# Kernel optimization log

Measured on AMD Instinct MI355X. Metric: run time of the kernel, lower is better.

## Reference

```python
import jax, jax.numpy as jnp
import numpy as np

EMBED_SIZE = 2048
EBS = 512            # embed_block_size
NB = EMBED_SIZE // EBS  # num_blocks = 4
HEADS = 8
HD = EBS // HEADS    # head_dim = 64
N, S = 4, 1024


def block_linear(x, W, b):
    # x: [T, NB, EBS], W: [NB, EBS, EBS], b: [NB, EBS]
    return jnp.einsum('tbi,bio->tbo', x, W) + b


def setup_inputs() -> dict:
    key = jax.random.key(0)
    ks = jax.random.split(key, 11)
    sc = 1.0 / np.sqrt(EBS)
    inp = {
        'values': jax.random.normal(ks[0], (N, S, EMBED_SIZE), jnp.float32),
        'keys': jax.random.normal(ks[1], (N, S, EMBED_SIZE), jnp.float32),
        'query': jax.random.normal(ks[2], (N, S, EMBED_SIZE), jnp.float32),
        'mask': jnp.ones((N, 1, 1, S, S), jnp.int32),
        'Wv': jax.random.normal(ks[3], (NB, EBS, EBS), jnp.float32) * sc,
        'bv': jnp.zeros((NB, EBS), jnp.float32),
        'Wk': jax.random.normal(ks[4], (NB, EBS, EBS), jnp.float32) * sc,
        'bk': jnp.zeros((NB, EBS), jnp.float32),
        'Wq': jax.random.normal(ks[5], (NB, EBS, EBS), jnp.float32) * sc,
        'bq': jnp.zeros((NB, EBS), jnp.float32),
        'Wo': jax.random.normal(ks[6], (NB, EBS, EBS), jnp.float32) * sc,
        'bo': jnp.zeros((NB, EBS), jnp.float32),
    }
    return inp


def reference(values, keys, query, mask, Wv, bv, Wk, bk, Wq, bq, Wo, bo):
    n, ql = query.shape[0], query.shape[1]
    vl, kl = values.shape[1], keys.shape[1]
    # block-diagonal QKV projections
    v = block_linear(values.reshape(-1, NB, EBS), Wv, bv)
    k = block_linear(keys.reshape(-1, NB, EBS), Wk, bk)
    q = block_linear(query.reshape(-1, NB, EBS), Wq, bq)
    v = v.reshape(n, vl, NB, HEADS, HD)
    k = k.reshape(n, kl, NB, HEADS, HD)
    q = q.reshape(n, ql, NB, HEADS, HD)
    energy = jnp.einsum('nqbhd,nkbhd->nbhqk', q, k)
    energy = jnp.where(mask == 0, jnp.float32(-1e20), energy)
    # NOTE: faithful to original: softmax over dim=3 (the query axis of nbhqk)
    attention = jax.nn.softmax(energy / np.sqrt(HD), axis=3)
    out = jnp.einsum('nbhql,nlbhd->nqbhd', attention, v)
    out = out.reshape(n * ql, NB, HEADS * HD)
    out = block_linear(out, Wo, bo)
    return out.reshape(n, ql, -1)
```

## Files before the change

### kernel.cpp

```cpp
#include <hip/hip_runtime.h>


typedef unsigned short u16;
typedef __bf16 bf16x8 __attribute__((ext_vector_type(8)));
typedef float f32x4 __attribute__((ext_vector_type(4)));

#define S_LEN 1024
#define HD 64
#define EMB 2048
#define EBS 512
#define C2EXP 0.18033688011112042f

__device__ __forceinline__ u16 f2b(float f) {
    union { float f; unsigned int i; } x; x.f = f;
    return (u16)((x.i + 0x8000u) >> 16);
}
__device__ __forceinline__ float b2f(u16 u) {
    union { unsigned int i; float f; } x; x.i = ((unsigned int)u) << 16;
    return x.f;
}
__device__ __forceinline__ bf16x8 ld8(const u16* p) {
    return *reinterpret_cast<const bf16x8*>(p);
}

__device__ __forceinline__ int dtype_probe(const void* src, int tid, int* s_flag) {
    if (tid < 64) {
        u16 v = ((const u16*)src)[tid * 2];
        int e = (v >> 7) & 0xFF;
        int sane = (e >= 117 && e <= 134);
        unsigned long long b = __ballot(sane);
        if (tid == 0) *s_flag = (__popcll(b) < 32) ? 1 : 0;
    }
    __syncthreads();
    return *s_flag;
}

__global__ __launch_bounds__(256) void wtrans(
    const void* __restrict__ Wv, const void* __restrict__ Wk,
    const void* __restrict__ Wq, const void* __restrict__ Wo,
    u16* __restrict__ WT, const void* __restrict__ probe)
{
    const int p = blockIdx.z >> 2, b = blockIdx.z & 3;
    const void* Wp = (p == 0 ? Wv : p == 1 ? Wk : p == 2 ? Wq : Wo);
    const size_t boff = (size_t)b * EBS * EBS;
    u16* D = WT + (size_t)(p * 4 + b) * EBS * EBS;
    const int i0 = blockIdx.x * 64, o0 = blockIdx.y * 64;
    const int tid = threadIdx.x;
    __shared__ __align__(16) u16 tile[64][72];
    __shared__ int s_flag;
    const int is32 = dtype_probe(probe, tid, &s_flag);
    for (int c = tid; c < 512; c += 256) {
        const int r = c >> 3, c8 = (c & 7) << 3;
        union { uint4 v; u16 u[8]; } pk;
        if (is32) {
            const float* src = (const float*)Wp + boff + (size_t)(i0 + r) * EBS + o0 + c8;
            const float4 f0 = *(const float4*)src, f1 = *(const float4*)(src + 4);
            pk.u[0] = f2b(f0.x); pk.u[1] = f2b(f0.y); pk.u[2] = f2b(f0.z); pk.u[3] = f2b(f0.w);
            pk.u[4] = f2b(f1.x); pk.u[5] = f2b(f1.y); pk.u[6] = f2b(f1.z); pk.u[7] = f2b(f1.w);
        } else {
            pk.v = *(const uint4*)((const u16*)Wp + boff + (size_t)(i0 + r) * EBS + o0 + c8);
        }
        *(uint4*)&tile[r][c8] = pk.v;
    }
    __syncthreads();
    for (int c = tid; c < 512; c += 256) {
        const int r = c >> 3, c8 = (c & 7) << 3;
        union { uint4 v; u16 u[8]; } pk;
        #pragma unroll
        for (int j = 0; j < 8; ++j) pk.u[j] = tile[c8 + j][r];
        *(uint4*)(D + (size_t)(o0 + r) * EBS + i0 + c8) = pk.v;
    }
}

__global__ __launch_bounds__(256) void gemm_qkv(
    const void* __restrict__ A, const void* __restrict__ W, const u16* __restrict__ WTp,
    const void* __restrict__ bias, u16* __restrict__ dst,
    const void* __restrict__ probe, int use_wt, int vmode, float oscale)
{
    const int tm = blockIdx.x, tn = blockIdx.y, b = blockIdx.z;
    const int tid = threadIdx.x;
    const int wave = tid >> 6, lane = tid & 63, quad = lane >> 4, c16 = lane & 15;
    const int wm = wave >> 1, wn = wave & 1;

    __shared__ __align__(16) u16 Al[128 * 40];
    __shared__ __align__(16) u16 Bl[128 * 40];
    __shared__ int s_flag;
    const int is32 = dtype_probe(probe, tid, &s_flag);

    f32x4 acc[4][4];
    #pragma unroll
    for (int i = 0; i < 4; ++i)
        #pragma unroll
        for (int j = 0; j < 4; ++j) acc[i][j] = (f32x4){0.f, 0.f, 0.f, 0.f};

    const size_t aoff = (size_t)tm * 128 * EMB + (size_t)b * EBS;
    const u16*   Ab = (const u16*)A + aoff;
    const float* Af = (const float*)A + aoff;
    const size_t woff = (size_t)b * EBS * EBS + (size_t)tn * 128;
    const u16*   Wb = (const u16*)W + woff;
    const float* Wf = (const float*)W + woff;
    const u16*   Tb = WTp + (size_t)b * EBS * EBS + (size_t)tn * 128 * EBS;

    for (int k0 = 0; k0 < EBS; k0 += 32) {
        for (int c = tid; c < 512; c += 256) {
            const int r = c >> 2, c8 = (c & 3) << 3;
            if (is32) {
                const float* p = Af + (size_t)r * EMB + k0 + c8;
                const float4 f0 = *(const float4*)p, f1 = *(const float4*)(p + 4);
                union { uint4 v; u16 u[8]; } pk;
                pk.u[0] = f2b(f0.x); pk.u[1] = f2b(f0.y); pk.u[2] = f2b(f0.z); pk.u[3] = f2b(f0.w);
                pk.u[4] = f2b(f1.x); pk.u[5] = f2b(f1.y); pk.u[6] = f2b(f1.z); pk.u[7] = f2b(f1.w);
                *(uint4*)&Al[r * 40 + c8] = pk.v;
            } else {
                *(uint4*)&Al[r * 40 + c8] = *(const uint4*)(Ab + (size_t)r * EMB + k0 + c8);
            }
        }
        if (use_wt) {
            for (int c = tid; c < 512; c += 256) {
                const int r = c >> 2, c8 = (c & 3) << 3;
                *(uint4*)&Bl[r * 40 + c8] = *(const uint4*)(Tb + (size_t)r * EBS + k0 + c8);
            }
        } else {
            for (int c = tid; c < 512; c += 256) {
                const int i = c & 31, oc = c >> 5;
                u16 h[8];
                if (is32) {
                    const float* p = Wf + (size_t)(k0 + i) * EBS + oc * 8;
                    const float4 f0 = *(const float4*)p, f1 = *(const float4*)(p + 4);
                    h[0] = f2b(f0.x); h[1] = f2b(f0.y); h[2] = f2b(f0.z); h[3] = f2b(f0.w);
                    h[4] = f2b(f1.x); h[5] = f2b(f1.y); h[6] = f2b(f1.z); h[7] = f2b(f1.w);
                } else {
                    union { uint4 v; u16 u[8]; } pk;
                    pk.v = *(const uint4*)(Wb + (size_t)(k0 + i) * EBS + oc * 8);
                    #pragma unroll
                    for (int j = 0; j < 8; ++j) h[j] = pk.u[j];
                }
                #pragma unroll
                for (int j = 0; j < 8; ++j) Bl[(oc * 8 + j) * 40 + i] = h[j];
            }
        }
        __syncthreads();
        bf16x8 af[4], bfr[4];
        #pragma unroll
        for (int ms = 0; ms < 4; ++ms)
            af[ms] = ld8(&Al[(wm * 64 + ms * 16 + c16) * 40 + quad * 8]);
        #pragma unroll
        for (int ns = 0; ns < 4; ++ns)
            bfr[ns] = ld8(&Bl[(wn * 64 + ns * 16 + c16) * 40 + quad * 8]);
        if (vmode == 0) {
            #pragma unroll
            for (int ms = 0; ms < 4; ++ms)
                #pragma unroll
                for (int ns = 0; ns < 4; ++ns)
                    acc[ms][ns] = __builtin_amdgcn_mfma_f32_16x16x32_bf16(af[ms], bfr[ns], acc[ms][ns], 0, 0, 0);
        } else {
            #pragma unroll
            for (int ms = 0; ms < 4; ++ms)
                #pragma unroll
                for (int ns = 0; ns < 4; ++ns)
                    acc[ms][ns] = __builtin_amdgcn_mfma_f32_16x16x32_bf16(bfr[ns], af[ms], acc[ms][ns], 0, 0, 0);
        }
        __syncthreads();
    }

    if (vmode == 0) {
        #pragma unroll
        for (int ns = 0; ns < 4; ++ns) {
            const int o = tn * 128 + wn * 64 + ns * 16 + c16;
            const float bb = is32 ? ((const float*)bias)[b * EBS + o]
                                  : b2f(((const u16*)bias)[b * EBS + o]);
            #pragma unroll
            for (int ms = 0; ms < 4; ++ms) {
                #pragma unroll
                for (int r = 0; r < 4; ++r) {
                    const int t = tm * 128 + wm * 64 + ms * 16 + quad * 4 + r;
                    const int n = t >> 10, s = t & 1023;
                    const int h = o >> 6, d = o & 63;
                    const int hid = (n * 4 + b) * 8 + h;
                    dst[(size_t)hid * (S_LEN * HD) + (size_t)s * HD + d] = f2b((acc[ms][ns][r] + bb) * oscale);
                }
            }
        }
    } else {
        #pragma unroll
        for (int ns = 0; ns < 4; ++ns) {
            #pragma unroll
            for (int r = 0; r < 4; ++r) {
                const int o = tn * 128 + wn * 64 + ns * 16 + quad * 4 + r;
                const float bb = is32 ? ((const float*)bias)[b * EBS + o]
                                      : b2f(((const u16*)bias)[b * EBS + o]);
                const int h = o >> 6, d = o & 63;
                #pragma unroll
                for (int ms = 0; ms < 4; ++ms) {
                    const int t = tm * 128 + wm * 64 + ms * 16 + c16;
                    const int n = t >> 10, s = t & 1023;
                    const int hid = (n * 4 + b) * 8 + h;
                    dst[(size_t)hid * (S_LEN * HD) + (size_t)d * S_LEN + s] = f2b((acc[ms][ns][r] + bb) * oscale);
                }
            }
        }
    }
}

__global__ __launch_bounds__(256) void attn_colstats(
    const u16* __restrict__ qws, const u16* __restrict__ kws,
    float* __restrict__ logs2)
{
    const int hid = blockIdx.x, lb = blockIdx.y;
    const int tid = threadIdx.x;
    const int wave = tid >> 6, lane = tid & 63, quad = lane >> 4, c16 = lane & 15;
    const int l0 = lb * 128;

    __shared__ __align__(16) u16 Ql[64 * 72];

    const u16* Kp = kws + (size_t)hid * (S_LEN * HD);
    const u16* Qp = qws + (size_t)hid * (S_LEN * HD);

    bf16x8 ak[2][2];
    #pragma unroll
    for (int s = 0; s < 2; ++s) {
        const size_t row = (size_t)(l0 + s * 64 + wave * 16 + c16) * HD;
        ak[s][0] = ld8(&Kp[row + quad * 8]);
        ak[s][1] = ld8(&Kp[row + 32 + quad * 8]);
    }

    float sum[2][4];
    #pragma unroll
    for (int s = 0; s < 2; ++s)
        #pragma unroll
        for (int r = 0; r < 4; ++r) sum[s][r] = 0.f;

    for (int q0 = 0; q0 < S_LEN; q0 += 64) {
        for (int c = tid; c < 512; c += 256) {
            const int r = c >> 3, c8 = (c & 7) << 3;
            *(uint4*)&Ql[r * 72 + c8] = *(const uint4*)(Qp + (size_t)(q0 + r) * HD + c8);
        }
        __syncthreads();
        #pragma unroll
        for (int qs = 0; qs < 4; ++qs) {
            const bf16x8 bq0 = ld8(&Ql[(qs * 16 + c16) * 72 + quad * 8]);
            const bf16x8 bq1 = ld8(&Ql[(qs * 16 + c16) * 72 + 32 + quad * 8]);
            #pragma unroll
            for (int s = 0; s < 2; ++s) {
                f32x4 e = (f32x4){0.f, 0.f, 0.f, 0.f};
                e = __builtin_amdgcn_mfma_f32_16x16x32_bf16(ak[s][0], bq0, e, 0, 0, 0);
                e = __builtin_amdgcn_mfma_f32_16x16x32_bf16(ak[s][1], bq1, e, 0, 0, 0);
                #pragma unroll
                for (int r = 0; r < 4; ++r)
                    sum[s][r] += exp2f(e[r]);
            }
        }
        __syncthreads();
    }
    #pragma unroll
    for (int s = 0; s < 2; ++s) {
        #pragma unroll
        for (int r = 0; r < 4; ++r) {
            float ss = sum[s][r];
            ss += __shfl_xor(ss, 1);
            ss += __shfl_xor(ss, 2);
            ss += __shfl_xor(ss, 4);
            ss += __shfl_xor(ss, 8);
            if (c16 == 0) {
                const int l = l0 + s * 64 + wave * 16 + quad * 4 + r;
                logs2[hid * S_LEN + l] = log2f(ss);
            }
        }
    }
}

__global__ __launch_bounds__(256) void attn_pass2(
    const u16* __restrict__ qws, const u16* __restrict__ kws, const u16* __restrict__ vws,
    const float* __restrict__ logs2,
    u16* __restrict__ omid, float* __restrict__ dout, int out32)
{
    const int hid = blockIdx.x, qb = blockIdx.y;
    const int tid = threadIdx.x;
    const int wave = tid >> 6, lane = tid & 63, quad = lane >> 4, c16 = lane & 15;
    const int q0 = qb * 128;

    __shared__ __align__(16) u16 Kl[64 * 72];
    __shared__ __align__(16) u16 Vt[64 * 72];
    __shared__ __align__(16) u16 Pl[4][32 * 72];
    __shared__ float lt[64];

    const u16* Qp  = qws + (size_t)hid * (S_LEN * HD);
    const u16* Kp  = kws + (size_t)hid * (S_LEN * HD);
    const u16* VpT = vws + (size_t)hid * (S_LEN * HD);

    bf16x8 aq[2][2];
    #pragma unroll
    for (int s = 0; s < 2; ++s) {
        const size_t row = (size_t)(q0 + s * 64 + wave * 16 + c16) * HD;
        aq[s][0] = ld8(&Qp[row + quad * 8]);
        aq[s][1] = ld8(&Qp[row + 32 + quad * 8]);
    }

    f32x4 oacc[2][4];
    #pragma unroll
    for (int s = 0; s < 2; ++s)
        #pragma unroll
        for (int i = 0; i < 4; ++i) oacc[s][i] = (f32x4){0.f, 0.f, 0.f, 0.f};

    for (int l0 = 0; l0 < S_LEN; l0 += 64) {
        for (int c = tid; c < 512; c += 256) {
            const int r = c >> 3, c8 = (c & 7) << 3;
            *(uint4*)&Kl[r * 72 + c8] = *(const uint4*)(Kp + (size_t)(l0 + r) * HD + c8);
        }
        for (int c = tid; c < 512; c += 256) {
            const int r = c >> 3, c8 = (c & 7) << 3;
            *(uint4*)&Vt[r * 72 + c8] = *(const uint4*)(VpT + (size_t)r * S_LEN + l0 + c8);
        }
        if (tid < 64) lt[tid] = logs2[hid * S_LEN + l0 + tid];
        __syncthreads();

        #pragma unroll
        for (int ls = 0; ls < 4; ++ls) {
            const bf16x8 bk0 = ld8(&Kl[(ls * 16 + c16) * 72 + quad * 8]);
            const bf16x8 bk1 = ld8(&Kl[(ls * 16 + c16) * 72 + 32 + quad * 8]);
            const int lcol = ls * 16 + c16;
            const float lg = lt[lcol];
            #pragma unroll
            for (int s = 0; s < 2; ++s) {
                f32x4 e = (f32x4){0.f, 0.f, 0.f, 0.f};
                e = __builtin_amdgcn_mfma_f32_16x16x32_bf16(aq[s][0], bk0, e, 0, 0, 0);
                e = __builtin_amdgcn_mfma_f32_16x16x32_bf16(aq[s][1], bk1, e, 0, 0, 0);
                #pragma unroll
                for (int r = 0; r < 4; ++r) {
                    const float p = exp2f(e[r] - lg);
                    Pl[wave][(s * 16 + quad * 4 + r) * 72 + lcol] = f2b(p);
                }
            }
        }
        __syncthreads();

        bf16x8 ap[2][2];
        #pragma unroll
        for (int s = 0; s < 2; ++s) {
            ap[s][0] = ld8(&Pl[wave][(s * 16 + c16) * 72 + quad * 8]);
            ap[s][1] = ld8(&Pl[wave][(s * 16 + c16) * 72 + 32 + quad * 8]);
        }
        #pragma unroll
        for (int ns = 0; ns < 4; ++ns) {
            const bf16x8 bv0 = ld8(&Vt[(ns * 16 + c16) * 72 + quad * 8]);
            const bf16x8 bv1 = ld8(&Vt[(ns * 16 + c16) * 72 + 32 + quad * 8]);
            #pragma unroll
            for (int s = 0; s < 2; ++s) {
                oacc[s][ns] = __builtin_amdgcn_mfma_f32_16x16x32_bf16(ap[s][0], bv0, oacc[s][ns], 0, 0, 0);
                oacc[s][ns] = __builtin_amdgcn_mfma_f32_16x16x32_bf16(ap[s][1], bv1, oacc[s][ns], 0, 0, 0);
            }
        }
        __syncthreads();
    }

    const int nn = hid >> 5, bb = (hid >> 3) & 3, hh = hid & 7;
    #pragma unroll
    for (int s = 0; s < 2; ++s) {
        #pragma unroll
        for (int ns = 0; ns < 4; ++ns) {
            #pragma unroll
            for (int r = 0; r < 4; ++r) {
                const int q = q0 + s * 64 + wave * 16 + quad * 4 + r;
                const int d = ns * 16 + c16;
                const size_t idx = (size_t)(nn * 1024 + q) * EMB + bb * EBS + hh * HD + d;
                if (out32) dout[idx] = oacc[s][ns][r];
                else       omid[idx] = f2b(oacc[s][ns][r]);
            }
        }
    }
}

__global__ __launch_bounds__(256) void gemm_final_wt(
    const u16* __restrict__ omid, const u16* __restrict__ WTo,
    const void* __restrict__ bias, float* __restrict__ C,
    const void* __restrict__ probe)
{
    const int tm = blockIdx.x, tn = blockIdx.y, b = blockIdx.z;
    const int tid = threadIdx.x;
    const int wave = tid >> 6, lane = tid & 63, quad = lane >> 4, c16 = lane & 15;
    const int wm = wave >> 1, wn = wave & 1;

    __shared__ __align__(16) u16 Al[128 * 40];
    __shared__ __align__(16) u16 Bl[128 * 40];
    __shared__ int s_flag;
    const int is32 = dtype_probe(probe, tid, &s_flag);

    f32x4 acc[4][4];
    #pragma unroll
    for (int i = 0; i < 4; ++i)
        #pragma unroll
        for (int j = 0; j < 4; ++j) acc[i][j] = (f32x4){0.f, 0.f, 0.f, 0.f};

    const u16* Ab = omid + (size_t)tm * 128 * EMB + (size_t)b * EBS;
    const u16* Tb = WTo + (size_t)b * EBS * EBS + (size_t)tn * 128 * EBS;

    for (int k0 = 0; k0 < EBS; k0 += 32) {
        for (int c = tid; c < 512; c += 256) {
            const int r = c >> 2, c8 = (c & 3) << 3;
            *(uint4*)&Al[r * 40 + c8] = *(const uint4*)(Ab + (size_t)r * EMB + k0 + c8);
        }
        for (int c = tid; c < 512; c += 256) {
            const int r = c >> 2, c8 = (c & 3) << 3;
            *(uint4*)&Bl[r * 40 + c8] = *(const uint4*)(Tb + (size_t)r * EBS + k0 + c8);
        }
        __syncthreads();
        bf16x8 af[4], bfr[4];
        #pragma unroll
        for (int ms = 0; ms < 4; ++ms)
            af[ms] = ld8(&Al[(wm * 64 + ms * 16 + c16) * 40 + quad * 8]);
        #pragma unroll
        for (int ns = 0; ns < 4; ++ns)
            bfr[ns] = ld8(&Bl[(wn * 64 + ns * 16 + c16) * 40 + quad * 8]);
        #pragma unroll
        for (int ms = 0; ms < 4; ++ms)
            #pragma unroll
            for (int ns = 0; ns < 4; ++ns)
                acc[ms][ns] = __builtin_amdgcn_mfma_f32_16x16x32_bf16(af[ms], bfr[ns], acc[ms][ns], 0, 0, 0);
        __syncthreads();
    }

    #pragma unroll
    for (int ns = 0; ns < 4; ++ns) {
        const int o = tn * 128 + wn * 64 + ns * 16 + c16;
        const float bb = is32 ? ((const float*)bias)[b * EBS + o]
                              : b2f(((const u16*)bias)[b * EBS + o]);
        #pragma unroll
        for (int ms = 0; ms < 4; ++ms) {
            #pragma unroll
            for (int r = 0; r < 4; ++r) {
                const int t = tm * 128 + wm * 64 + ms * 16 + quad * 4 + r;
                C[(size_t)t * EMB + (size_t)b * EBS + o] = acc[ms][ns][r] + bb;
            }
        }
    }
}

__global__ __launch_bounds__(1024) void gemm_final_inplace(
    float* __restrict__ C, const void* __restrict__ W, const void* __restrict__ bias,
    const void* __restrict__ probe)
{
    const int tm = blockIdx.x, b = blockIdx.y;
    const int tid = threadIdx.x;
    const int wave = tid >> 6, lane = tid & 63, quad = lane >> 4, c16 = lane & 15;
    const int wm = wave >> 3, wn = wave & 7;

    __shared__ __align__(16) u16 Al[128 * 40];
    __shared__ __align__(16) u16 Bl[512 * 40];
    __shared__ int s_flag;
    const int is32 = dtype_probe(probe, tid, &s_flag);

    f32x4 acc[4][4];
    #pragma unroll
    for (int i = 0; i < 4; ++i)
        #pragma unroll
        for (int j = 0; j < 4; ++j) acc[i][j] = (f32x4){0.f, 0.f, 0.f, 0.f};

    const float* Ab = C + (size_t)tm * 128 * EMB + (size_t)b * EBS;
    const u16*   Wb = (const u16*)W + (size_t)b * EBS * EBS;
    const float* Wf = (const float*)W + (size_t)b * EBS * EBS;

    for (int k0 = 0; k0 < EBS; k0 += 32) {
        for (int c = tid; c < 512; c += 1024) {
            const int r = c >> 2, c8 = (c & 3) << 3;
            const float* p = Ab + (size_t)r * EMB + k0 + c8;
            const float4 f0 = *(const float4*)p, f1 = *(const float4*)(p + 4);
            union { uint4 v; u16 u[8]; } pk;
            pk.u[0] = f2b(f0.x); pk.u[1] = f2b(f0.y); pk.u[2] = f2b(f0.z); pk.u[3] = f2b(f0.w);
            pk.u[4] = f2b(f1.x); pk.u[5] = f2b(f1.y); pk.u[6] = f2b(f1.z); pk.u[7] = f2b(f1.w);
            *(uint4*)&Al[r * 40 + c8] = pk.v;
        }
        for (int c = tid; c < 2048; c += 1024) {
            const int i = c & 31, oc = c >> 5;
            u16 h[8];
            if (is32) {
                const float* p = Wf + (size_t)(k0 + i) * EBS + oc * 8;
                const float4 f0 = *(const float4*)p, f1 = *(const float4*)(p + 4);
                h[0] = f2b(f0.x); h[1] = f2b(f0.y); h[2] = f2b(f0.z); h[3] = f2b(f0.w);
                h[4] = f2b(f1.x); h[5] = f2b(f1.y); h[6] = f2b(f1.z); h[7] = f2b(f1.w);
            } else {
                union { uint4 v; u16 u[8]; } pk;
                pk.v = *(const uint4*)(Wb + (size_t)(k0 + i) * EBS + oc * 8);
                #pragma unroll
                for (int j = 0; j < 8; ++j) h[j] = pk.u[j];
            }
            #pragma unroll
            for (int j = 0; j < 8; ++j) Bl[(oc * 8 + j) * 40 + i] = h[j];
        }
        __syncthreads();
        bf16x8 af[4], bfr[4];
        #pragma unroll
        for (int ms = 0; ms < 4; ++ms)
            af[ms] = ld8(&Al[(wm * 64 + ms * 16 + c16) * 40 + quad * 8]);
        #pragma unroll
        for (int ns = 0; ns < 4; ++ns)
            bfr[ns] = ld8(&Bl[(wn * 64 + ns * 16 + c16) * 40 + quad * 8]);
        #pragma unroll
        for (int ms = 0; ms < 4; ++ms)
            #pragma unroll
            for (int ns = 0; ns < 4; ++ns)
                acc[ms][ns] = __builtin_amdgcn_mfma_f32_16x16x32_bf16(af[ms], bfr[ns], acc[ms][ns], 0, 0, 0);
        __syncthreads();
    }

    #pragma unroll
    for (int ns = 0; ns < 4; ++ns) {
        const int o = wn * 64 + ns * 16 + c16;
        const float bb = is32 ? ((const float*)bias)[b * EBS + o]
                              : b2f(((const u16*)bias)[b * EBS + o]);
        #pragma unroll
        for (int ms = 0; ms < 4; ++ms) {
            #pragma unroll
            for (int r = 0; r < 4; ++r) {
                const int t = tm * 128 + wm * 64 + ms * 16 + quad * 4 + r;
                C[(size_t)t * EMB + (size_t)b * EBS + o] = acc[ms][ns][r] + bb;
            }
        }
    }
}

extern "C" void kernel_launch(void* const* d_in, const int* in_sizes, int n_in,
                              void* d_out, int out_size, void* d_ws, size_t ws_size,
                              hipStream_t stream)
{
    (void)in_sizes; (void)n_in; (void)out_size;

    const void* values = d_in[0];
    const void* keys   = d_in[1];
    const void* query  = d_in[2];
    const void* Wv = d_in[4];  const void* bv = d_in[5];
    const void* Wk = d_in[6];  const void* bk = d_in[7];
    const void* Wq = d_in[8];  const void* bq = d_in[9];
    const void* Wo = d_in[10]; const void* bo = d_in[11];

    char* ws = (char*)d_ws;
    u16* qws = (u16*)(ws);
    u16* kws = (u16*)(ws + (16ull << 20));
    u16* vws = (u16*)(ws + (32ull << 20));
    float* out = (float*)d_out;

    const bool full = ws_size >= (73ull << 20);

    if (full) {
        u16* omid  = (u16*)(ws + (48ull << 20));
        u16* WT    = (u16*)(ws + (64ull << 20));
        float* logs2 = (float*)(ws + (72ull << 20));
        u16* WTv = WT;
        u16* WTk = WT + (1u << 20);
        u16* WTq = WT + (2u << 20);
        u16* WTo = WT + (3u << 20);

        wtrans<<<dim3(8, 8, 16), 256, 0, stream>>>(Wv, Wk, Wq, Wo, WT, values);
        gemm_qkv<<<dim3(32, 4, 4), 256, 0, stream>>>(values, Wv, WTv, bv, vws, values, 1, 1, 1.0f);
        gemm_qkv<<<dim3(32, 4, 4), 256, 0, stream>>>(keys,   Wk, WTk, bk, kws, values, 1, 0, 1.0f);
        gemm_qkv<<<dim3(32, 4, 4), 256, 0, stream>>>(query,  Wq, WTq, bq, qws, values, 1, 0, C2EXP);
        attn_colstats<<<dim3(128, 8), 256, 0, stream>>>(qws, kws, logs2);
        attn_pass2<<<dim3(128, 8), 256, 0, stream>>>(qws, kws, vws, logs2, omid, out, 0);
        gemm_final_wt<<<dim3(32, 4, 4), 256, 0, stream>>>(omid, WTo, bo, out, values);
    } else {
        float* logs2 = (float*)(ws + (48ull << 20));
        gemm_qkv<<<dim3(32, 4, 4), 256, 0, stream>>>(values, Wv, (const u16*)Wv, bv, vws, values, 0, 1, 1.0f);
        gemm_qkv<<<dim3(32, 4, 4), 256, 0, stream>>>(keys,   Wk, (const u16*)Wk, bk, kws, values, 0, 0, 1.0f);
        gemm_qkv<<<dim3(32, 4, 4), 256, 0, stream>>>(query,  Wq, (const u16*)Wq, bq, qws, values, 0, 0, C2EXP);
        attn_colstats<<<dim3(128, 8), 256, 0, stream>>>(qws, kws, logs2);
        attn_pass2<<<dim3(128, 8), 256, 0, stream>>>(qws, kws, vws, logs2, (u16*)out, out, 1);
        gemm_final_inplace<<<dim3(32, 4), 1024, 0, stream>>>(out, Wo, bo, values);
    }
}
```

Baseline: 416.1 us.

## Fold softmax column normalisation into V projection and swizzle attention LDS

The per-key softmax normaliser (1/sum) is now computed before the V projection and multiplied into V in the projection epilogue. The attention pass then needs only exp2 of the logits, with no per-column log subtraction and no lt shared table. LDS tiles drop the padded stride of 72 for an XOR-swizzled stride of 64. The MFMA operands are swapped so each lane writes four packed bf16 probabilities as one 8-byte store, and the syncthreads between the P write and P read is removed because each wave owns its own P buffer. The risk is lower precision, since V is now rounded to bf16 after scaling, and the V GEMM must wait for colstats.

```diff
diff --git a/kernel.cpp b/kernel.cpp
--- a/kernel.cpp
+++ b/kernel.cpp
@@ -21,6 +21,13 @@
 }
 __device__ __forceinline__ bf16x8 ld8(const u16* p) {
     return *reinterpret_cast<const bf16x8*>(p);
+}
+__device__ __forceinline__ unsigned int pack2(float a, float b) {
+    union { float f; unsigned int i; } x, y; x.f = a; y.f = b;
+    return ((x.i + 0x8000u) >> 16) | ((y.i + 0x8000u) & 0xFFFF0000u);
+}
+__device__ __forceinline__ int swz(int r, int c) {
+    return (r << 6) + (c ^ ((r & 7) << 3));
 }
 
 __device__ __forceinline__ int dtype_probe(const void* src, int tid, int* s_flag) {
@@ -75,7 +82,8 @@
 __global__ __launch_bounds__(256) void gemm_qkv(
     const void* __restrict__ A, const void* __restrict__ W, const u16* __restrict__ WTp,
     const void* __restrict__ bias, u16* __restrict__ dst,
-    const void* __restrict__ probe, int use_wt, int vmode, float oscale)
+    const void* __restrict__ probe, int use_wt, int vmode, float oscale,
+    const float* __restrict__ vsc)
 {
     const int tm = blockIdx.x, tn = blockIdx.y, b = blockIdx.z;
     const int tid = threadIdx.x;
@@ -195,7 +203,9 @@
                     const int t = tm * 128 + wm * 64 + ms * 16 + c16;
                     const int n = t >> 10, s = t & 1023;
                     const int hid = (n * 4 + b) * 8 + h;
-                    dst[(size_t)hid * (S_LEN * HD) + (size_t)d * S_LEN + s] = f2b((acc[ms][ns][r] + bb) * oscale);
+                    float val = (acc[ms][ns][r] + bb) * oscale;
+                    if (vsc) val *= vsc[(size_t)hid * S_LEN + s];
+                    dst[(size_t)hid * (S_LEN * HD) + (size_t)d * S_LEN + s] = f2b(val);
                 }
             }
         }
@@ -204,7 +214,7 @@
 
 __global__ __launch_bounds__(256) void attn_colstats(
     const u16* __restrict__ qws, const u16* __restrict__ kws,
-    float* __restrict__ logs2)
+    float* __restrict__ vscale)
 {
     const int hid = blockIdx.x, lb = blockIdx.y;
     const int tid = threadIdx.x;
@@ -263,7 +273,7 @@
             ss += __shfl_xor(ss, 8);
             if (c16 == 0) {
                 const int l = l0 + s * 64 + wave * 16 + quad * 4 + r;
-                logs2[hid * S_LEN + l] = log2f(ss);
+                vscale[hid * S_LEN + l] = 1.0f / ss;
             }
         }
     }
@@ -271,7 +281,6 @@
 
 __global__ __launch_bounds__(256) void attn_pass2(
     const u16* __restrict__ qws, const u16* __restrict__ kws, const u16* __restrict__ vws,
-    const float* __restrict__ logs2,
     u16* __restrict__ omid, float* __restrict__ dout, int out32)
 {
     const int hid = blockIdx.x, qb = blockIdx.y;
@@ -279,14 +288,14 @@
     const int wave = tid >> 6, lane = tid & 63, quad = lane >> 4, c16 = lane & 15;
     const int q0 = qb * 128;
 
-    __shared__ __align__(16) u16 Kl[64 * 72];
-    __shared__ __align__(16) u16 Vt[64 * 72];
-    __shared__ __align__(16) u16 Pl[4][32 * 72];
-    __shared__ float lt[64];
+    __shared__ __align__(16) u16 Kl[64 * 64];
+    __shared__ __align__(16) u16 Vt[64 * 64];
+    __shared__ __align__(16) u16 Pl[4][32 * 64];
 
     const u16* Qp  = qws + (size_t)hid * (S_LEN * HD);
     const u16* Kp  = kws + (size_t)hid * (S_LEN * HD);
     const u16* VpT = vws + (size_t)hid * (S_LEN * HD);
+    u16* Pw = &Pl[wave][0];
 
     bf16x8 aq[2][2];
     #pragma unroll
@@ -305,45 +314,41 @@
     for (int l0 = 0; l0 < S_LEN; l0 += 64) {
         for (int c = tid; c < 512; c += 256) {
             const int r = c >> 3, c8 = (c & 7) << 3;
-            *(uint4*)&Kl[r * 72 + c8] = *(const uint4*)(Kp + (size_t)(l0 + r) * HD + c8);
+            *(uint4*)&Kl[swz(r, c8)] = *(const uint4*)(Kp + (size_t)(l0 + r) * HD + c8);
         }
         for (int c = tid; c < 512; c += 256) {
             const int r = c >> 3, c8 = (c & 7) << 3;
-            *(uint4*)&Vt[r * 72 + c8] = *(const uint4*)(VpT + (size_t)r * S_LEN + l0 + c8);
-        }
-        if (tid < 64) lt[tid] = logs2[hid * S_LEN + l0 + tid];
+            *(uint4*)&Vt[swz(r, c8)] = *(const uint4*)(VpT + (size_t)r * S_LEN + l0 + c8);
+        }
         __syncthreads();
 
         #pragma unroll
         for (int ls = 0; ls < 4; ++ls) {
-            const bf16x8 bk0 = ld8(&Kl[(ls * 16 + c16) * 72 + quad * 8]);
-            const bf16x8 bk1 = ld8(&Kl[(ls * 16 + c16) * 72 + 32 + quad * 8]);
-            const int lcol = ls * 16 + c16;
-            const float lg = lt[lcol];
+            const int lr = ls * 16 + c16;
+            const bf16x8 ak0 = ld8(&Kl[swz(lr, quad * 8)]);
+            const bf16x8 ak1 = ld8(&Kl[swz(lr, 32 + quad * 8)]);
             #pragma unroll
             for (int s = 0; s < 2; ++s) {
                 f32x4 e = (f32x4){0.f, 0.f, 0.f, 0.f};
-                e = __builtin_amdgcn_mfma_f32_16x16x32_bf16(aq[s][0], bk0, e, 0, 0, 0);
-                e = __builtin_amdgcn_mfma_f32_16x16x32_bf16(aq[s][1], bk1, e, 0, 0, 0);
-                #pragma unroll
-                for (int r = 0; r < 4; ++r) {
-                    const float p = exp2f(e[r] - lg);
-                    Pl[wave][(s * 16 + quad * 4 + r) * 72 + lcol] = f2b(p);
-                }
-            }
-        }
-        __syncthreads();
+                e = __builtin_amdgcn_mfma_f32_16x16x32_bf16(ak0, aq[s][0], e, 0, 0, 0);
+                e = __builtin_amdgcn_mfma_f32_16x16x32_bf16(ak1, aq[s][1], e, 0, 0, 0);
+                union { uint2 v; unsigned int w[2]; } pp;
+                pp.w[0] = pack2(exp2f(e[0]), exp2f(e[1]));
+                pp.w[1] = pack2(exp2f(e[2]), exp2f(e[3]));
+                *(uint2*)&Pw[swz(s * 16 + c16, ls * 16 + quad * 4)] = pp.v;
+            }
+        }
 
         bf16x8 ap[2][2];
         #pragma unroll
         for (int s = 0; s < 2; ++s) {
-            ap[s][0] = ld8(&Pl[wave][(s * 16 + c16) * 72 + quad * 8]);
-            ap[s][1] = ld8(&Pl[wave][(s * 16 + c16) * 72 + 32 + quad * 8]);
+            ap[s][0] = ld8(&Pw[swz(s * 16 + c16, quad * 8)]);
+            ap[s][1] = ld8(&Pw[swz(s * 16 + c16, 32 + quad * 8)]);
         }
         #pragma unroll
         for (int ns = 0; ns < 4; ++ns) {
-            const bf16x8 bv0 = ld8(&Vt[(ns * 16 + c16) * 72 + quad * 8]);
-            const bf16x8 bv1 = ld8(&Vt[(ns * 16 + c16) * 72 + 32 + quad * 8]);
+            const bf16x8 bv0 = ld8(&Vt[swz(ns * 16 + c16, quad * 8)]);
+            const bf16x8 bv1 = ld8(&Vt[swz(ns * 16 + c16, 32 + quad * 8)]);
             #pragma unroll
             for (int s = 0; s < 2; ++s) {
                 oacc[s][ns] = __builtin_amdgcn_mfma_f32_16x16x32_bf16(ap[s][0], bv0, oacc[s][ns], 0, 0, 0);
@@ -543,26 +548,26 @@
     if (full) {
         u16* omid  = (u16*)(ws + (48ull << 20));
         u16* WT    = (u16*)(ws + (64ull << 20));
-        float* logs2 = (float*)(ws + (72ull << 20));
+        float* vscale = (float*)(ws + (72ull << 20));
         u16* WTv = WT;
         u16* WTk = WT + (1u << 20);
         u16* WTq = WT + (2u << 20);
         u16* WTo = WT + (3u << 20);
 
         wtrans<<<dim3(8, 8, 16), 256, 0, stream>>>(Wv, Wk, Wq, Wo, WT, values);
-        gemm_qkv<<<dim3(32, 4, 4), 256, 0, stream>>>(values, Wv, WTv, bv, vws, values, 1, 1, 1.0f);
-        gemm_qkv<<<dim3(32, 4, 4), 256, 0, stream>>>(keys,   Wk, WTk, bk, kws, values, 1, 0, 1.0f);
-        gemm_qkv<<<dim3(32, 4, 4), 256, 0, stream>>>(query,  Wq, WTq, bq, qws, values, 1, 0, C2EXP);
-        attn_colstats<<<dim3(128, 8), 256, 0, stream>>>(qws, kws, logs2);
-        attn_pass2<<<dim3(128, 8), 256, 0, stream>>>(qws, kws, vws, logs2, omid, out, 0);
+        gemm_qkv<<<dim3(32, 4, 4), 256, 0, stream>>>(keys,   Wk, WTk, bk, kws, values, 1, 0, 1.0f, nullptr);
+        gemm_qkv<<<dim3(32, 4, 4), 256, 0, stream>>>(query,  Wq, WTq, bq, qws, values, 1, 0, C2EXP, nullptr);
+        attn_colstats<<<dim3(128, 8), 256, 0, stream>>>(qws, kws, vscale);
+        gemm_qkv<<<dim3(32, 4, 4), 256, 0, stream>>>(values, Wv, WTv, bv, vws, values, 1, 1, 1.0f, vscale);
+        attn_pass2<<<dim3(128, 8), 256, 0, stream>>>(qws, kws, vws, omid, out, 0);
         gemm_final_wt<<<dim3(32, 4, 4), 256, 0, stream>>>(omid, WTo, bo, out, values);
     } else {
-        float* logs2 = (float*)(ws + (48ull << 20));
-        gemm_qkv<<<dim3(32, 4, 4), 256, 0, stream>>>(values, Wv, (const u16*)Wv, bv, vws, values, 0, 1, 1.0f);
-        gemm_qkv<<<dim3(32, 4, 4), 256, 0, stream>>>(keys,   Wk, (const u16*)Wk, bk, kws, values, 0, 0, 1.0f);
-        gemm_qkv<<<dim3(32, 4, 4), 256, 0, stream>>>(query,  Wq, (const u16*)Wq, bq, qws, values, 0, 0, C2EXP);
-        attn_colstats<<<dim3(128, 8), 256, 0, stream>>>(qws, kws, logs2);
-        attn_pass2<<<dim3(128, 8), 256, 0, stream>>>(qws, kws, vws, logs2, (u16*)out, out, 1);
+        float* vscale = (float*)(ws + (48ull << 20));
+        gemm_qkv<<<dim3(32, 4, 4), 256, 0, stream>>>(keys,   Wk, (const u16*)Wk, bk, kws, values, 0, 0, 1.0f, nullptr);
+        gemm_qkv<<<dim3(32, 4, 4), 256, 0, stream>>>(query,  Wq, (const u16*)Wq, bq, qws, values, 0, 0, C2EXP, nullptr);
+        attn_colstats<<<dim3(128, 8), 256, 0, stream>>>(qws, kws, vscale);
+        gemm_qkv<<<dim3(32, 4, 4), 256, 0, stream>>>(values, Wv, (const u16*)Wv, bv, vws, values, 0, 1, 1.0f, vscale);
+        attn_pass2<<<dim3(128, 8), 256, 0, stream>>>(qws, kws, vws, (u16*)out, out, 1);
         gemm_final_inplace<<<dim3(32, 4), 1024, 0, stream>>>(out, Wo, bo, values);
     }
 }
```

Measured after the change: 423.3 us. No clear change (+1.7%).
